# Performance work log

Measured on AMD Instinct MI355X. Metric: run time of the kernel, lower is better.

The kernel has to match this reference:

```python
import jax, jax.numpy as jnp
import numpy as np
import math

N_HEADS = 8
FACTOR = 1


def setup_inputs() -> dict:
    key = jax.random.key(0)
    k1, k2, k3 = jax.random.split(key, 3)
    B, L, E = 16, 2048, 512
    return {
        "queries": jax.random.normal(k1, (B, L, E), dtype=jnp.float32),
        "keys": jax.random.normal(k2, (B, L, E), dtype=jnp.float32),
        "values": jax.random.normal(k3, (B, L, E), dtype=jnp.float32),
        "attn_mask": jnp.zeros((1,), dtype=bool),  # unused by the original forward
    }


def _time_delay_agg(values, corr, factor):
    # values, corr: (B, H, L, C)
    B, H, L, C = values.shape
    top_k = max(1, int(factor * math.log(L)))
    # NOTE: topk over the last (channel) axis, faithfully matching the source.
    weights, delay = jax.lax.top_k(corr, top_k)          # (B,H,L,K)
    weights = jax.nn.softmax(weights, axis=-1)
    positions = jnp.arange(L).reshape(1, 1, L, 1)
    delay_idx = (positions - delay) % L                   # (B,H,L,K), time indices
    idx = delay_idx.reshape(B, H, L * top_k, 1)
    gathered = jnp.take_along_axis(values, idx, axis=2)   # (B,H,L*K,C)
    gathered = gathered.reshape(B, H, L, top_k, C)
    return (gathered * weights[..., None]).sum(axis=3)    # (B,H,L,C)


def reference(queries, keys, values, attn_mask):
    B, L, E = queries.shape
    _, S, _ = values.shape
    H = N_HEADS
    hd = E // H
    q = queries.reshape(B, L, H, hd).transpose(0, 2, 1, 3)  # (B,H,L,hd)
    k = keys.reshape(B, S, H, hd).transpose(0, 2, 1, 3)
    v = values.reshape(B, S, H, hd).transpose(0, 2, 1, 3)
    if L > S:
        pad = L - S
        zeros = jnp.zeros((B, H, pad, hd), dtype=v.dtype)
        v = jnp.concatenate([v, zeros], axis=2)
        k = jnp.concatenate([k, zeros], axis=2)
    else:
        v = v[:, :, :L, :]
        k = k[:, :, :L, :]
    # period-based dependency discovery via FFT cross-correlation along time
    q_fft = jnp.fft.rfft(q, axis=2)
    k_fft = jnp.fft.rfft(k, axis=2)
    corr = jnp.fft.irfft(q_fft * jnp.conj(k_fft), n=L, axis=2)  # (B,H,L,hd)
    out = _time_delay_agg(v, corr, FACTOR)                       # (B,H,L,hd)
    return out.transpose(0, 2, 1, 3).reshape(B, L, E)
```

## Files before the change

### kernel.cpp

```cpp
#include <hip/hip_runtime.h>
#include <math.h>

#define LEN   2048
#define EDIM  512
#define NB    16
#define NH    8
#define HD    64
#define TOPK  7
#define NXCD  8
#define LBLK  64

__device__ inline float2 cmul(float2 a, float2 b) {
    return make_float2(a.x * b.x - a.y * b.y, a.x * b.y + a.y * b.x);
}
__device__ inline float2 cadd(float2 a, float2 b) { return make_float2(a.x + b.x, a.y + b.y); }
__device__ inline float2 csub(float2 a, float2 b) { return make_float2(a.x - b.x, a.y - b.y); }
__device__ inline int sw(int i) { return i ^ ((i >> 5) & 15); }

__device__ inline float2 cexp_rev(float r) {
    return make_float2(__builtin_amdgcn_cosf(r), __builtin_amdgcn_sinf(r));
}

__device__ inline void tw8r(float r, float2* w) {
    w[1] = cexp_rev(r);
    w[2] = cmul(w[1], w[1]);
    w[3] = cmul(w[2], w[1]);
    w[4] = cmul(w[2], w[2]);
    w[5] = cmul(w[3], w[2]);
    w[6] = cmul(w[3], w[3]);
    w[7] = cmul(w[4], w[3]);
}

__device__ inline void fwd8(float2* P, int base, int stride, const float2* w) {
    const float C = 0.70710678118654752f;
    float2 v[8];
    #pragma unroll
    for (int r = 0; r < 8; ++r) v[r] = P[sw(base + stride * r)];
    float2 y0 = cadd(v[0], v[4]), y1 = cadd(v[1], v[5]);
    float2 y2 = cadd(v[2], v[6]), y3 = cadd(v[3], v[7]);
    float2 t0 = csub(v[0], v[4]), t1 = csub(v[1], v[5]);
    float2 t2 = csub(v[2], v[6]), t3 = csub(v[3], v[7]);
    float2 z0 = t0;
    float2 z1 = make_float2(C * (t1.x + t1.y), C * (t1.y - t1.x));
    float2 z2 = make_float2(t2.y, -t2.x);
    float2 z3 = make_float2(C * (t3.y - t3.x), -C * (t3.x + t3.y));
    float2 a0 = cadd(y0, y2), a1 = cadd(y1, y3);
    float2 b0 = csub(y0, y2), tb = csub(y1, y3);
    float2 b1 = make_float2(tb.y, -tb.x);
    float2 c0 = cadd(z0, z2), c1 = cadd(z1, z3);
    float2 d0 = csub(z0, z2), td = csub(z1, z3);
    float2 d1 = make_float2(td.y, -td.x);
    float2 X0 = cadd(a0, a1), X4 = csub(a0, a1);
    float2 X2 = cadd(b0, b1), X6 = csub(b0, b1);
    float2 X1 = cadd(c0, c1), X5 = csub(c0, c1);
    float2 X3 = cadd(d0, d1), X7 = csub(d0, d1);
    P[sw(base)]              = X0;
    P[sw(base + stride)]     = cmul(X1, w[1]);
    P[sw(base + 2 * stride)] = cmul(X2, w[2]);
    P[sw(base + 3 * stride)] = cmul(X3, w[3]);
    P[sw(base + 4 * stride)] = cmul(X4, w[4]);
    P[sw(base + 5 * stride)] = cmul(X5, w[5]);
    P[sw(base + 6 * stride)] = cmul(X6, w[6]);
    P[sw(base + 7 * stride)] = cmul(X7, w[7]);
}

__device__ inline void fwd8nt(float2* P, int base) {
    const float C = 0.70710678118654752f;
    float2 v[8];
    #pragma unroll
    for (int r = 0; r < 8; ++r) v[r] = P[sw(base + r)];
    float2 y0 = cadd(v[0], v[4]), y1 = cadd(v[1], v[5]);
    float2 y2 = cadd(v[2], v[6]), y3 = cadd(v[3], v[7]);
    float2 t0 = csub(v[0], v[4]), t1 = csub(v[1], v[5]);
    float2 t2 = csub(v[2], v[6]), t3 = csub(v[3], v[7]);
    float2 z0 = t0;
    float2 z1 = make_float2(C * (t1.x + t1.y), C * (t1.y - t1.x));
    float2 z2 = make_float2(t2.y, -t2.x);
    float2 z3 = make_float2(C * (t3.y - t3.x), -C * (t3.x + t3.y));
    float2 a0 = cadd(y0, y2), a1 = cadd(y1, y3);
    float2 b0 = csub(y0, y2), tb = csub(y1, y3);
    float2 b1 = make_float2(tb.y, -tb.x);
    float2 c0 = cadd(z0, z2), c1 = cadd(z1, z3);
    float2 d0 = csub(z0, z2), td = csub(z1, z3);
    float2 d1 = make_float2(td.y, -td.x);
    P[sw(base)]     = cadd(a0, a1);
    P[sw(base + 4)] = csub(a0, a1);
    P[sw(base + 2)] = cadd(b0, b1);
    P[sw(base + 6)] = csub(b0, b1);
    P[sw(base + 1)] = cadd(c0, c1);
    P[sw(base + 5)] = csub(c0, c1);
    P[sw(base + 3)] = cadd(d0, d1);
    P[sw(base + 7)] = csub(d0, d1);
}

__device__ inline void inv8(float2* P, int base, int stride, const float2* w) {
    const float C = 0.70710678118654752f;
    float2 v[8];
    #pragma unroll
    for (int p = 0; p < 8; ++p) v[p] = P[sw(base + stride * p)];
    #pragma unroll
    for (int p = 1; p < 8; ++p) v[p] = cmul(v[p], w[p]);
    float2 y0 = cadd(v[0], v[4]), y1 = cadd(v[1], v[5]);
    float2 y2 = cadd(v[2], v[6]), y3 = cadd(v[3], v[7]);
    float2 t0 = csub(v[0], v[4]), t1 = csub(v[1], v[5]);
    float2 t2 = csub(v[2], v[6]), t3 = csub(v[3], v[7]);
    float2 z0 = t0;
    float2 z1 = make_float2(C * (t1.x - t1.y), C * (t1.x + t1.y));
    float2 z2 = make_float2(-t2.y, t2.x);
    float2 z3 = make_float2(-C * (t3.x + t3.y), C * (t3.x - t3.y));
    float2 a0 = cadd(y0, y2), a1 = cadd(y1, y3);
    float2 b0 = csub(y0, y2), tb = csub(y1, y3);
    float2 b1 = make_float2(-tb.y, tb.x);
    float2 c0 = cadd(z0, z2), c1 = cadd(z1, z3);
    float2 d0 = csub(z0, z2), td = csub(z1, z3);
    float2 d1 = make_float2(-td.y, td.x);
    P[sw(base)]              = cadd(a0, a1);
    P[sw(base + 4 * stride)] = csub(a0, a1);
    P[sw(base + 2 * stride)] = cadd(b0, b1);
    P[sw(base + 6 * stride)] = csub(b0, b1);
    P[sw(base + stride)]     = cadd(c0, c1);
    P[sw(base + 5 * stride)] = csub(c0, c1);
    P[sw(base + 3 * stride)] = cadd(d0, d1);
    P[sw(base + 7 * stride)] = csub(d0, d1);
}

__device__ inline void inv8nt(float2* P, int base) {
    const float C = 0.70710678118654752f;
    float2 v[8];
    #pragma unroll
    for (int p = 0; p < 8; ++p) v[p] = P[sw(base + p)];
    float2 y0 = cadd(v[0], v[4]), y1 = cadd(v[1], v[5]);
    float2 y2 = cadd(v[2], v[6]), y3 = cadd(v[3], v[7]);
    float2 t0 = csub(v[0], v[4]), t1 = csub(v[1], v[5]);
    float2 t2 = csub(v[2], v[6]), t3 = csub(v[3], v[7]);
    float2 z0 = t0;
    float2 z1 = make_float2(C * (t1.x - t1.y), C * (t1.x + t1.y));
    float2 z2 = make_float2(-t2.y, t2.x);
    float2 z3 = make_float2(-C * (t3.x + t3.y), C * (t3.x - t3.y));
    float2 a0 = cadd(y0, y2), a1 = cadd(y1, y3);
    float2 b0 = csub(y0, y2), tb = csub(y1, y3);
    float2 b1 = make_float2(-tb.y, tb.x);
    float2 c0 = cadd(z0, z2), c1 = cadd(z1, z3);
    float2 d0 = csub(z0, z2), td = csub(z1, z3);
    float2 d1 = make_float2(-td.y, td.x);
    P[sw(base)]     = cadd(a0, a1);
    P[sw(base + 4)] = csub(a0, a1);
    P[sw(base + 2)] = cadd(b0, b1);
    P[sw(base + 6)] = csub(b0, b1);
    P[sw(base + 1)] = cadd(c0, c1);
    P[sw(base + 5)] = csub(c0, c1);
    P[sw(base + 3)] = cadd(d0, d1);
    P[sw(base + 7)] = csub(d0, d1);
}

__device__ inline void fwd4s(float2* P, int j) {
    float2 v0 = P[sw(j)], v1 = P[sw(j + 512)], v2 = P[sw(j + 1024)], v3 = P[sw(j + 1536)];
    float2 a0 = cadd(v0, v2), a1 = cadd(v1, v3);
    float2 b0 = csub(v0, v2), t = csub(v1, v3);
    float2 b1 = make_float2(t.y, -t.x);
    float2 X0 = cadd(a0, a1), X2 = csub(a0, a1);
    float2 X1 = cadd(b0, b1), X3 = csub(b0, b1);
    float2 w1 = cexp_rev(-(float)j * (1.0f / 2048.0f));
    float2 w2 = cmul(w1, w1);
    float2 w3 = cmul(w2, w1);
    P[sw(j)]        = X0;
    P[sw(j + 512)]  = cmul(X1, w1);
    P[sw(j + 1024)] = cmul(X2, w2);
    P[sw(j + 1536)] = cmul(X3, w3);
}
__device__ inline void inv4s(float2* P, int j) {
    float2 v0 = P[sw(j)], v1 = P[sw(j + 512)], v2 = P[sw(j + 1024)], v3 = P[sw(j + 1536)];
    float2 w1 = cexp_rev((float)j * (1.0f / 2048.0f));
    float2 w2 = cmul(w1, w1);
    float2 w3 = cmul(w2, w1);
    v1 = cmul(v1, w1); v2 = cmul(v2, w2); v3 = cmul(v3, w3);
    float2 a0 = cadd(v0, v2), a1 = cadd(v1, v3);
    float2 b0 = csub(v0, v2), t = csub(v1, v3);
    float2 b1 = make_float2(-t.y, t.x);
    P[sw(j)]        = cadd(a0, a1);
    P[sw(j + 1024)] = csub(a0, a1);
    P[sw(j + 512)]  = cadd(b0, b1);
    P[sw(j + 1536)] = csub(b0, b1);
}

__device__ inline int slotOf(int k) {
    return ((k & 3) << 9) | (((k >> 2) & 7) << 6) | (((k >> 5) & 7) << 3) | ((k >> 8) & 7);
}

__device__ inline void fft_core(float2* A, float2* Bs, int tid) {
    int lane  = tid & 63;
    int chunk = (tid >> 6) << 9;
    float2 w[8];

    fwd4s(A, tid);  fwd4s(A, tid + 256);
    fwd4s(Bs, tid); fwd4s(Bs, tid + 256);
    __syncthreads();

    tw8r(-(float)lane * (1.0f / 512.0f), w);
    fwd8(A,  chunk + lane, 64, w);
    fwd8(Bs, chunk + lane, 64, w);
    {
        int base = chunk + ((lane >> 3) << 6) + (lane & 7);
        tw8r(-(float)(lane & 7) * (1.0f / 64.0f), w);
        fwd8(A,  base, 8, w);
        fwd8(Bs, base, 8, w);
    }
    fwd8nt(A,  chunk + (lane << 3));
    fwd8nt(Bs, chunk + (lane << 3));
    __syncthreads();

    for (int f = tid; f <= 1024; f += 256) {
        int nf = (2048 - f) & 2047;
        int ia = sw(slotOf(f));
        int ib = sw(slotOf(nf));
        float2 z1 = A[ia],  z1n = A[ib];
        float2 z2 = Bs[ia], z2n = Bs[ib];
        float Qx = 0.5f * (z1.x + z1n.x), Qy = 0.5f * (z1.y - z1n.y);
        float Kx = 0.5f * (z1.y + z1n.y), Ky = 0.5f * (z1n.x - z1.x);
        float C1x = Qx * Kx + Qy * Ky;
        float C1y = Qy * Kx - Qx * Ky;
        float Px = 0.5f * (z2.x + z2n.x), Py = 0.5f * (z2.y - z2n.y);
        float Lx = 0.5f * (z2.y + z2n.y), Ly = 0.5f * (z2n.x - z2.x);
        float C2x = Px * Lx + Py * Ly;
        float C2y = Py * Lx - Px * Ly;
        A[ia] = make_float2(C1x - C2y, C1y + C2x);
        if (f != 0 && f != 1024)
            A[ib] = make_float2(C1x + C2y, C2x - C1y);
    }
    __syncthreads();

    inv8nt(A, chunk + (lane << 3));
    {
        int base = chunk + ((lane >> 3) << 6) + (lane & 7);
        tw8r((float)(lane & 7) * (1.0f / 64.0f), w);
        inv8(A, base, 8, w);
    }
    tw8r((float)lane * (1.0f / 512.0f), w);
    inv8(A, chunk + lane, 64, w);
    __syncthreads();

    inv4s(A, tid); inv4s(A, tid + 256);
    __syncthreads();
}

__global__ __launch_bounds__(256) void fft_corr_strided(const float* __restrict__ q,
                                                        const float* __restrict__ k,
                                                        float* __restrict__ corr,
                                                        int chStart) {
    __shared__ float2 A[LEN];
    __shared__ float2 Bs[LEN];
    int bid = blockIdx.x;
    int nwg = gridDim.x;
    int cp  = ((nwg & (NXCD - 1)) == 0) ? (bid & (NXCD - 1)) * (nwg >> 3) + (bid >> 3)
                                        : bid;
    int chLocal = cp * 2;
    int gch = chStart + chLocal;
    int b   = gch >> 9;
    int e   = gch & (EDIM - 1);
    int tid = threadIdx.x;
    const float* qr = q + (size_t)b * LEN * EDIM + e;
    const float* kr = k + (size_t)b * LEN * EDIM + e;
    #pragma unroll
    for (int j = 0; j < LEN / 256; ++j) {
        int t = tid + 256 * j;
        float2 qv = *(const float2*)(qr + (size_t)t * EDIM);
        float2 kv = *(const float2*)(kr + (size_t)t * EDIM);
        A[sw(t)]  = make_float2(qv.x, kv.x);
        Bs[sw(t)] = make_float2(qv.y, kv.y);
    }
    __syncthreads();
    fft_core(A, Bs, tid);
    const float inv = 1.0f / (float)LEN;
    float4* c0 = (float4*)(corr + (size_t)chLocal * LEN);
    float4* c1 = (float4*)(corr + (size_t)(chLocal + 1) * LEN);
    for (int t4 = tid; t4 < LEN / 4; t4 += 256) {
        int t = t4 * 4;
        float2 e0 = A[sw(t)], e1 = A[sw(t + 1)], e2 = A[sw(t + 2)], e3 = A[sw(t + 3)];
        c0[t4] = make_float4(e0.x * inv, e1.x * inv, e2.x * inv, e3.x * inv);
        c1[t4] = make_float4(e0.y * inv, e1.y * inv, e2.y * inv, e3.y * inv);
    }
}

__global__ __launch_bounds__(64) void topk_agg(const float* __restrict__ corr,
                                               const float* __restrict__ values,
                                               float* __restrict__ out,
                                               int bhBase) {
    __shared__ float2 w_d[LBLK][TOPK];
    int l0 = blockIdx.x * LBLK;
    int lh = blockIdx.y;
    int bh = bhBase + lh;
    int b  = bh >> 3;
    int h  = bh & 7;
    int tid = threadIdx.x;

    const float* cb = corr + (size_t)lh * HD * LEN + l0 + tid;
    float wk[TOPK];
    int   dk[TOPK];
    #pragma unroll
    for (int t = 0; t < TOPK; ++t) { wk[t] = -INFINITY; dk[t] = 0; }
    #pragma unroll 16
    for (int c = 0; c < HD; ++c) {
        float nv = cb[(size_t)c * LEN];
        int   nd = c;
        #pragma unroll
        for (int t = 0; t < TOPK; ++t) {
            bool  m  = nv > wk[t];
            float tv = wk[t]; int td = dk[t];
            wk[t] = m ? nv : tv;
            dk[t] = m ? nd : td;
            nv    = m ? tv : nv;
            nd    = m ? td : nd;
        }
    }
    float mx = wk[0], sum = 0.f;
    float e[TOPK];
    #pragma unroll
    for (int t = 0; t < TOPK; ++t) { e[t] = expf(wk[t] - mx); sum += e[t]; }
    float invs = 1.f / sum;
    #pragma unroll
    for (int t = 0; t < TOPK; ++t)
        w_d[tid][t] = make_float2(e[t] * invs, __int_as_float(dk[t]));
    __syncthreads();

    const float* vb = values + (size_t)b * LEN * EDIM + h * HD + tid;
    float*       ob = out    + (size_t)b * LEN * EDIM + h * HD + tid;
    for (int i0 = 0; i0 < LBLK; i0 += 4) {
        float acc0 = 0.f, acc1 = 0.f, acc2 = 0.f, acc3 = 0.f;
        int lb = l0 + i0;
        #pragma unroll
        for (int t = 0; t < TOPK; ++t) {
            float2 wd0 = w_d[i0 + 0][t];
            float2 wd1 = w_d[i0 + 1][t];
            float2 wd2 = w_d[i0 + 2][t];
            float2 wd3 = w_d[i0 + 3][t];
            int i0x = (lb + 0 - __float_as_int(wd0.y)) & (LEN - 1);
            int i1x = (lb + 1 - __float_as_int(wd1.y)) & (LEN - 1);
            int i2x = (lb + 2 - __float_as_int(wd2.y)) & (LEN - 1);
            int i3x = (lb + 3 - __float_as_int(wd3.y)) & (LEN - 1);
            acc0 += wd0.x * vb[(size_t)i0x * EDIM];
            acc1 += wd1.x * vb[(size_t)i1x * EDIM];
            acc2 += wd2.x * vb[(size_t)i2x * EDIM];
            acc3 += wd3.x * vb[(size_t)i3x * EDIM];
        }
        ob[(size_t)(lb + 0) * EDIM] = acc0;
        ob[(size_t)(lb + 1) * EDIM] = acc1;
        ob[(size_t)(lb + 2) * EDIM] = acc2;
        ob[(size_t)(lb + 3) * EDIM] = acc3;
    }
}

extern "C" void kernel_launch(void* const* d_in, const int* in_sizes, int n_in,
                              void* d_out, int out_size, void* d_ws, size_t ws_size,
                              hipStream_t stream) {
    const float* q = (const float*)d_in[0];
    const float* k = (const float*)d_in[1];
    const float* v = (const float*)d_in[2];
    float* out = (float*)d_out;

    const size_t CORR_BYTES = (size_t)NB * EDIM * LEN * sizeof(float);

    if (ws_size >= CORR_BYTES) {
        float* corr = (float*)d_ws;
        fft_corr_strided<<<dim3(NB * EDIM / 2), dim3(256), 0, stream>>>(q, k, corr, 0);
        topk_agg<<<dim3(LEN / LBLK, NB * NH), dim3(LBLK), 0, stream>>>(corr, v, out, 0);
    } else {
        const size_t HEAD_BYTES = (size_t)HD * LEN * sizeof(float);
        int headsPer = (int)(ws_size / HEAD_BYTES);
        if (headsPer < 1) headsPer = 1;
        if (headsPer > NB * NH) headsPer = NB * NH;
        float* corr = (float*)d_ws;
        for (int hs = 0; hs < NB * NH; hs += headsPer) {
            int hc = NB * NH - hs < headsPer ? NB * NH - hs : headsPer;
            fft_corr_strided<<<dim3(hc * HD / 2), dim3(256), 0, stream>>>(q, k, corr, hs * HD);
            topk_agg<<<dim3(LEN / LBLK, hc), dim3(LBLK), 0, stream>>>(corr, v, out, hs);
        }
    }
}
```

Before: 312.8 us.

## Restructure 2048-point shared-memory FFT as radix-16/16/8 stages

Replaces the radix-4 plus three radix-8 decomposition with two radix-16 passes and a final radix-8 pass for the forward FFT, and the mirror order for the inverse. Forward work is split so half the threads transform Q and half K, and the bin-slot mapping is changed to match. This cuts the number of shared-memory passes and twiddle computations. In exchange it adds extra barriers between stages that used to share a single warp-local sync, leaves half the threads idle during the inverse radix-16 passes, and raises register pressure with 16-element arrays.

```diff
diff --git a/kernel.cpp b/kernel.cpp
--- a/kernel.cpp
+++ b/kernel.cpp
@@ -21,47 +21,99 @@
     return make_float2(__builtin_amdgcn_cosf(r), __builtin_amdgcn_sinf(r));
 }
 
-__device__ inline void tw8r(float r, float2* w) {
-    w[1] = cexp_rev(r);
-    w[2] = cmul(w[1], w[1]);
-    w[3] = cmul(w[2], w[1]);
-    w[4] = cmul(w[2], w[2]);
-    w[5] = cmul(w[3], w[2]);
-    w[6] = cmul(w[3], w[3]);
-    w[7] = cmul(w[4], w[3]);
-}
-
-__device__ inline void fwd8(float2* P, int base, int stride, const float2* w) {
-    const float C = 0.70710678118654752f;
-    float2 v[8];
-    #pragma unroll
-    for (int r = 0; r < 8; ++r) v[r] = P[sw(base + stride * r)];
-    float2 y0 = cadd(v[0], v[4]), y1 = cadd(v[1], v[5]);
-    float2 y2 = cadd(v[2], v[6]), y3 = cadd(v[3], v[7]);
-    float2 t0 = csub(v[0], v[4]), t1 = csub(v[1], v[5]);
-    float2 t2 = csub(v[2], v[6]), t3 = csub(v[3], v[7]);
-    float2 z0 = t0;
-    float2 z1 = make_float2(C * (t1.x + t1.y), C * (t1.y - t1.x));
-    float2 z2 = make_float2(t2.y, -t2.x);
-    float2 z3 = make_float2(C * (t3.y - t3.x), -C * (t3.x + t3.y));
-    float2 a0 = cadd(y0, y2), a1 = cadd(y1, y3);
-    float2 b0 = csub(y0, y2), tb = csub(y1, y3);
-    float2 b1 = make_float2(tb.y, -tb.x);
-    float2 c0 = cadd(z0, z2), c1 = cadd(z1, z3);
-    float2 d0 = csub(z0, z2), td = csub(z1, z3);
-    float2 d1 = make_float2(td.y, -td.x);
-    float2 X0 = cadd(a0, a1), X4 = csub(a0, a1);
-    float2 X2 = cadd(b0, b1), X6 = csub(b0, b1);
-    float2 X1 = cadd(c0, c1), X5 = csub(c0, c1);
-    float2 X3 = cadd(d0, d1), X7 = csub(d0, d1);
-    P[sw(base)]              = X0;
-    P[sw(base + stride)]     = cmul(X1, w[1]);
-    P[sw(base + 2 * stride)] = cmul(X2, w[2]);
-    P[sw(base + 3 * stride)] = cmul(X3, w[3]);
-    P[sw(base + 4 * stride)] = cmul(X4, w[4]);
-    P[sw(base + 5 * stride)] = cmul(X5, w[5]);
-    P[sw(base + 6 * stride)] = cmul(X6, w[6]);
-    P[sw(base + 7 * stride)] = cmul(X7, w[7]);
+__device__ inline void fwd16(float2* P, int base, int stride, float2 w1) {
+    const float C1 = 0.9238795325112867f;
+    const float S1 = 0.3826834323650898f;
+    const float C2 = 0.7071067811865476f;
+    float2 v[16];
+    #pragma unroll
+    for (int r = 0; r < 16; ++r) v[r] = P[sw(base + stride * r)];
+    #pragma unroll
+    for (int j = 0; j < 4; ++j) {
+        float2 s02 = cadd(v[j], v[j + 8]),  d02 = csub(v[j], v[j + 8]);
+        float2 s13 = cadd(v[j + 4], v[j + 12]), d13 = csub(v[j + 4], v[j + 12]);
+        v[j]      = cadd(s02, s13);
+        v[j + 8]  = csub(s02, s13);
+        v[j + 4]  = make_float2(d02.x + d13.y, d02.y - d13.x);
+        v[j + 12] = make_float2(d02.x - d13.y, d02.y + d13.x);
+    }
+    v[5]  = cmul(v[5],  make_float2(C1, -S1));
+    v[6]  = cmul(v[6],  make_float2(C2, -C2));
+    v[7]  = cmul(v[7],  make_float2(S1, -C1));
+    v[9]  = cmul(v[9],  make_float2(C2, -C2));
+    v[10] = make_float2(v[10].y, -v[10].x);
+    v[11] = cmul(v[11], make_float2(-C2, -C2));
+    v[13] = cmul(v[13], make_float2(S1, -C1));
+    v[14] = cmul(v[14], make_float2(-C2, -C2));
+    v[15] = cmul(v[15], make_float2(-C1, S1));
+    float2 w2  = cmul(w1, w1);
+    float2 w4  = cmul(w2, w2);
+    float2 w8  = cmul(w4, w4);
+    float2 w12 = cmul(w8, w4);
+    float2 wpm = make_float2(1.f, 0.f);
+    #pragma unroll
+    for (int pm = 0; pm < 4; ++pm) {
+        float2 u0 = v[4 * pm], u1 = v[4 * pm + 1], u2 = v[4 * pm + 2], u3 = v[4 * pm + 3];
+        float2 s  = cadd(u0, u2), d  = csub(u0, u2);
+        float2 sp = cadd(u1, u3), dp = csub(u1, u3);
+        float2 X0 = cadd(s, sp);
+        float2 X2 = csub(s, sp);
+        float2 X1 = make_float2(d.x + dp.y, d.y - dp.x);
+        float2 X3 = make_float2(d.x - dp.y, d.y + dp.x);
+        P[sw(base + pm * stride)]        = cmul(X0, wpm);
+        P[sw(base + (pm + 4) * stride)]  = cmul(X1, cmul(wpm, w4));
+        P[sw(base + (pm + 8) * stride)]  = cmul(X2, cmul(wpm, w8));
+        P[sw(base + (pm + 12) * stride)] = cmul(X3, cmul(wpm, w12));
+        wpm = cmul(wpm, w1);
+    }
+}
+
+__device__ inline void inv16(float2* P, int base, int stride, float2 w1) {
+    const float C1 = 0.9238795325112867f;
+    const float S1 = 0.3826834323650898f;
+    const float C2 = 0.7071067811865476f;
+    float2 w2  = cmul(w1, w1);
+    float2 w4  = cmul(w2, w2);
+    float2 w8  = cmul(w4, w4);
+    float2 w12 = cmul(w8, w4);
+    float2 v[16];
+    float2 wpm = make_float2(1.f, 0.f);
+    #pragma unroll
+    for (int pm = 0; pm < 4; ++pm) {
+        v[pm]      = cmul(P[sw(base + pm * stride)], wpm);
+        v[pm + 4]  = cmul(P[sw(base + (pm + 4) * stride)], cmul(wpm, w4));
+        v[pm + 8]  = cmul(P[sw(base + (pm + 8) * stride)], cmul(wpm, w8));
+        v[pm + 12] = cmul(P[sw(base + (pm + 12) * stride)], cmul(wpm, w12));
+        wpm = cmul(wpm, w1);
+    }
+    #pragma unroll
+    for (int j = 0; j < 4; ++j) {
+        float2 s02 = cadd(v[j], v[j + 8]),  d02 = csub(v[j], v[j + 8]);
+        float2 s13 = cadd(v[j + 4], v[j + 12]), d13 = csub(v[j + 4], v[j + 12]);
+        v[j]      = cadd(s02, s13);
+        v[j + 8]  = csub(s02, s13);
+        v[j + 4]  = make_float2(d02.x - d13.y, d02.y + d13.x);
+        v[j + 12] = make_float2(d02.x + d13.y, d02.y - d13.x);
+    }
+    v[5]  = cmul(v[5],  make_float2(C1, S1));
+    v[6]  = cmul(v[6],  make_float2(C2, C2));
+    v[7]  = cmul(v[7],  make_float2(S1, C1));
+    v[9]  = cmul(v[9],  make_float2(C2, C2));
+    v[10] = make_float2(-v[10].y, v[10].x);
+    v[11] = cmul(v[11], make_float2(-C2, C2));
+    v[13] = cmul(v[13], make_float2(S1, C1));
+    v[14] = cmul(v[14], make_float2(-C2, C2));
+    v[15] = cmul(v[15], make_float2(-C1, -S1));
+    #pragma unroll
+    for (int rm = 0; rm < 4; ++rm) {
+        float2 u0 = v[4 * rm], u1 = v[4 * rm + 1], u2 = v[4 * rm + 2], u3 = v[4 * rm + 3];
+        float2 s  = cadd(u0, u2), d  = csub(u0, u2);
+        float2 sp = cadd(u1, u3), dp = csub(u1, u3);
+        P[sw(base + rm * stride)]        = cadd(s, sp);
+        P[sw(base + (rm + 8) * stride)]  = csub(s, sp);
+        P[sw(base + (rm + 4) * stride)]  = make_float2(d.x - dp.y, d.y + dp.x);
+        P[sw(base + (rm + 12) * stride)] = make_float2(d.x + dp.y, d.y - dp.x);
+    }
 }
 
 __device__ inline void fwd8nt(float2* P, int base) {
@@ -93,37 +145,6 @@
     P[sw(base + 7)] = csub(d0, d1);
 }
 
-__device__ inline void inv8(float2* P, int base, int stride, const float2* w) {
-    const float C = 0.70710678118654752f;
-    float2 v[8];
-    #pragma unroll
-    for (int p = 0; p < 8; ++p) v[p] = P[sw(base + stride * p)];
-    #pragma unroll
-    for (int p = 1; p < 8; ++p) v[p] = cmul(v[p], w[p]);
-    float2 y0 = cadd(v[0], v[4]), y1 = cadd(v[1], v[5]);
-    float2 y2 = cadd(v[2], v[6]), y3 = cadd(v[3], v[7]);
-    float2 t0 = csub(v[0], v[4]), t1 = csub(v[1], v[5]);
-    float2 t2 = csub(v[2], v[6]), t3 = csub(v[3], v[7]);
-    float2 z0 = t0;
-    float2 z1 = make_float2(C * (t1.x - t1.y), C * (t1.x + t1.y));
-    float2 z2 = make_float2(-t2.y, t2.x);
-    float2 z3 = make_float2(-C * (t3.x + t3.y), C * (t3.x - t3.y));
-    float2 a0 = cadd(y0, y2), a1 = cadd(y1, y3);
-    float2 b0 = csub(y0, y2), tb = csub(y1, y3);
-    float2 b1 = make_float2(-tb.y, tb.x);
-    float2 c0 = cadd(z0, z2), c1 = cadd(z1, z3);
-    float2 d0 = csub(z0, z2), td = csub(z1, z3);
-    float2 d1 = make_float2(-td.y, td.x);
-    P[sw(base)]              = cadd(a0, a1);
-    P[sw(base + 4 * stride)] = csub(a0, a1);
-    P[sw(base + 2 * stride)] = cadd(b0, b1);
-    P[sw(base + 6 * stride)] = csub(b0, b1);
-    P[sw(base + stride)]     = cadd(c0, c1);
-    P[sw(base + 5 * stride)] = csub(c0, c1);
-    P[sw(base + 3 * stride)] = cadd(d0, d1);
-    P[sw(base + 7 * stride)] = csub(d0, d1);
-}
-
 __device__ inline void inv8nt(float2* P, int base) {
     const float C = 0.70710678118654752f;
     float2 v[8];
@@ -153,66 +174,26 @@
     P[sw(base + 7)] = csub(d0, d1);
 }
 
-__device__ inline void fwd4s(float2* P, int j) {
-    float2 v0 = P[sw(j)], v1 = P[sw(j + 512)], v2 = P[sw(j + 1024)], v3 = P[sw(j + 1536)];
-    float2 a0 = cadd(v0, v2), a1 = cadd(v1, v3);
-    float2 b0 = csub(v0, v2), t = csub(v1, v3);
-    float2 b1 = make_float2(t.y, -t.x);
-    float2 X0 = cadd(a0, a1), X2 = csub(a0, a1);
-    float2 X1 = cadd(b0, b1), X3 = csub(b0, b1);
-    float2 w1 = cexp_rev(-(float)j * (1.0f / 2048.0f));
-    float2 w2 = cmul(w1, w1);
-    float2 w3 = cmul(w2, w1);
-    P[sw(j)]        = X0;
-    P[sw(j + 512)]  = cmul(X1, w1);
-    P[sw(j + 1024)] = cmul(X2, w2);
-    P[sw(j + 1536)] = cmul(X3, w3);
-}
-__device__ inline void inv4s(float2* P, int j) {
-    float2 v0 = P[sw(j)], v1 = P[sw(j + 512)], v2 = P[sw(j + 1024)], v3 = P[sw(j + 1536)];
-    float2 w1 = cexp_rev((float)j * (1.0f / 2048.0f));
-    float2 w2 = cmul(w1, w1);
-    float2 w3 = cmul(w2, w1);
-    v1 = cmul(v1, w1); v2 = cmul(v2, w2); v3 = cmul(v3, w3);
-    float2 a0 = cadd(v0, v2), a1 = cadd(v1, v3);
-    float2 b0 = csub(v0, v2), t = csub(v1, v3);
-    float2 b1 = make_float2(-t.y, t.x);
-    P[sw(j)]        = cadd(a0, a1);
-    P[sw(j + 1024)] = csub(a0, a1);
-    P[sw(j + 512)]  = cadd(b0, b1);
-    P[sw(j + 1536)] = csub(b0, b1);
-}
-
-__device__ inline int slotOf(int k) {
-    return ((k & 3) << 9) | (((k >> 2) & 7) << 6) | (((k >> 5) & 7) << 3) | ((k >> 8) & 7);
+__device__ inline int slotF(int k) {
+    return ((k & 15) << 7) | (((k >> 4) & 15) << 3) | ((k >> 8) & 7);
 }
 
 __device__ inline void fft_core(float2* A, float2* Bs, int tid) {
-    int lane  = tid & 63;
-    int chunk = (tid >> 6) << 9;
-    float2 w[8];
-
-    fwd4s(A, tid);  fwd4s(A, tid + 256);
-    fwd4s(Bs, tid); fwd4s(Bs, tid + 256);
-    __syncthreads();
-
-    tw8r(-(float)lane * (1.0f / 512.0f), w);
-    fwd8(A,  chunk + lane, 64, w);
-    fwd8(Bs, chunk + lane, 64, w);
-    {
-        int base = chunk + ((lane >> 3) << 6) + (lane & 7);
-        tw8r(-(float)(lane & 7) * (1.0f / 64.0f), w);
-        fwd8(A,  base, 8, w);
-        fwd8(Bs, base, 8, w);
-    }
-    fwd8nt(A,  chunk + (lane << 3));
-    fwd8nt(Bs, chunk + (lane << 3));
+    float2* P = (tid < 128) ? A : Bs;
+    int tt = tid & 127;
+
+    fwd16(P, tt, 128, cexp_rev(-(float)tt * (1.0f / 2048.0f)));
+    __syncthreads();
+    fwd16(P, ((tt >> 3) << 7) + (tt & 7), 8, cexp_rev(-(float)(tt & 7) * (1.0f / 128.0f)));
+    __syncthreads();
+    fwd8nt(P, tt << 4);
+    fwd8nt(P, (tt << 4) + 8);
     __syncthreads();
 
     for (int f = tid; f <= 1024; f += 256) {
         int nf = (2048 - f) & 2047;
-        int ia = sw(slotOf(f));
-        int ib = sw(slotOf(nf));
+        int ia = sw(slotF(f));
+        int ib = sw(slotF(nf));
         float2 z1 = A[ia],  z1n = A[ib];
         float2 z2 = Bs[ia], z2n = Bs[ib];
         float Qx = 0.5f * (z1.x + z1n.x), Qy = 0.5f * (z1.y - z1n.y);
@@ -229,17 +210,13 @@
     }
     __syncthreads();
 
-    inv8nt(A, chunk + (lane << 3));
-    {
-        int base = chunk + ((lane >> 3) << 6) + (lane & 7);
-        tw8r((float)(lane & 7) * (1.0f / 64.0f), w);
-        inv8(A, base, 8, w);
-    }
-    tw8r((float)lane * (1.0f / 512.0f), w);
-    inv8(A, chunk + lane, 64, w);
-    __syncthreads();
-
-    inv4s(A, tid); inv4s(A, tid + 256);
+    inv8nt(A, tid << 3);
+    __syncthreads();
+    if (tid < 128)
+        inv16(A, ((tid >> 3) << 7) + (tid & 7), 8, cexp_rev((float)(tid & 7) * (1.0f / 128.0f)));
+    __syncthreads();
+    if (tid < 128)
+        inv16(A, tid, 128, cexp_rev((float)tid * (1.0f / 2048.0f)));
     __syncthreads();
 }
 
```

Result: no change. 316.9 us (+1.3%).
